# Optimization experiments

Measured on AMD Instinct MI355X. Metric: run time of the kernel, lower is better.

Reference implementation:

```python
import jax, jax.numpy as jnp
import numpy as np

NUM_HEADS = 16
HEAD_DIM = 32  # out_ch 512 / 16 heads

def _c(x):
    # last axis holds (real, imag) -> complex64
    return jax.lax.complex(x[..., 0], x[..., 1])

def setup_inputs() -> dict:
    key = jax.random.key(0)
    ks = jax.random.split(key, 9)
    B, S, C = 1, 2048, 512
    mk = lambda k, shp: jax.random.normal(k, shp, dtype=jnp.float32)
    return {
        "Q": mk(ks[0], (B, S, C, 2)),
        "V": mk(ks[1], (B, S, C, 2)),
        "K": mk(ks[2], (B, S, C, 2)),
        "Wq": mk(ks[3], (C, C, 2)) * (1.0 / np.sqrt(C)),
        "bq": mk(ks[4], (C, 2)) * 0.02,
        "Wk": mk(ks[5], (C, C, 2)) * (1.0 / np.sqrt(C)),
        "bk": mk(ks[6], (C, 2)) * 0.02,
        "Wv": mk(ks[7], (C, C, 2)) * (1.0 / np.sqrt(C)),
        "bv": mk(ks[8], (C, 2)) * 0.02,
    }

def _split_heads(x):
    B, S, D = x.shape
    return x.reshape(B, S, NUM_HEADS, HEAD_DIM).transpose(0, 2, 1, 3)  # [B,H,S,d]

def reference(Q, V, K, Wq, bq, Wk, bk, Wv, bv):
    Qc, Kc, Vc = _c(Q), _c(K), _c(V)
    # torch Linear: y = x @ W^T + b, W is [out, in]
    proj = lambda x, W, b: jnp.einsum('bsi,oi->bso', x, _c(W)) + _c(b)
    q = _split_heads(proj(Qc, Wq, bq))  # [B,H,S,d] complex64
    k = _split_heads(proj(Kc, Wk, bk))
    v = _split_heads(proj(Vc, Wv, bv))
    scores = jnp.einsum('bhqd,bhkd->bhqk', q, jnp.conj(k)) / np.sqrt(HEAD_DIM).astype(np.float32)
    weights = jax.nn.softmax(jnp.abs(scores), axis=-1)  # real [B,H,S,S]
    out = jnp.einsum('bhqk,bhkd->bhqd', weights.astype(v.dtype), v)  # complex
    B, H, S, d = out.shape
    out = out.transpose(0, 2, 1, 3).reshape(B, S, H * d)  # [B,S,out_ch]
    return jnp.stack([out.real, out.imag], axis=-1)  # [B,S,out_ch,2] float32
```

## Files before the change

### kernel.cpp

```cpp
#include <hip/hip_runtime.h>
#include <hip/hip_bf16.h>
#include <math.h>

#define S_LEN 2048
#define C_DIM 512
#define NH 16
#define HD 32
#define PLANE_U (NH * S_LEN * HD)
#define XF_OFF  (6*(size_t)PLANE_U)
#define WF_OFF  (12*(size_t)PLANE_U)
#define WPLF 262144

typedef __attribute__((ext_vector_type(8)))  short bf16x8;
typedef __attribute__((ext_vector_type(4)))  float f32x4;
typedef __attribute__((ext_vector_type(16))) float f32x16;
typedef __attribute__((ext_vector_type(4)))  unsigned int u32x4;

#if __has_builtin(__builtin_amdgcn_exp2f)
#define EXP2(x) __builtin_amdgcn_exp2f(x)
#else
#define EXP2(x) exp2f(x)
#endif

__device__ __forceinline__ unsigned int pk_bf16(float a, float b) {
    float2 f; f.x = a; f.y = b;
    __hip_bfloat162 t = __float22bfloat162_rn(f);
    return *reinterpret_cast<unsigned int*>(&t);
}

__global__ __launch_bounds__(256)
void xcvt(const float* __restrict__ Q, const float* __restrict__ K,
          const float* __restrict__ V, unsigned short* __restrict__ ws)
{
    const int tid  = blockIdx.x*256 + threadIdx.x;
    const int z    = tid >> 17;
    const int rem  = tid & 131071;
    const int kidx = rem >> 11;
    const int s    = rem & 2047;
    const int k    = kidx * 8;
    const float2* x2 = (const float2*)(z == 0 ? Q : (z == 1 ? K : V));
    const float4* s4 = (const float4*)(x2 + (size_t)s*C_DIM + k);
    float4 f0 = s4[0], f1 = s4[1], f2v = s4[2], f3 = s4[3];
    u32x4 rh, ih;
    rh[0] = pk_bf16(f0.x, f0.z); rh[1] = pk_bf16(f1.x, f1.z);
    rh[2] = pk_bf16(f2v.x, f2v.z); rh[3] = pk_bf16(f3.x, f3.z);
    ih[0] = pk_bf16(f0.y, f0.w); ih[1] = pk_bf16(f1.y, f1.w);
    ih[2] = pk_bf16(f2v.y, f2v.w); ih[3] = pk_bf16(f3.y, f3.w);
    const int sb = s >> 4, lr = s & 15, g = kidx & 3, kc = kidx >> 2;
    const size_t off = ((size_t)(sb*16 + kc)*64 + g*16 + lr)*8;
    unsigned short* base = ws + XF_OFF + (size_t)z*2*PLANE_U;
    *(u32x4*)&base[off]           = rh;
    *(u32x4*)&base[PLANE_U + off] = ih;
}

__global__ __launch_bounds__(256)
void wcvt(const float* __restrict__ Wq, const float* __restrict__ Wk,
          const float* __restrict__ Wv, unsigned short* __restrict__ ws)
{
    const int tid  = blockIdx.x*256 + threadIdx.x;
    const int z    = tid >> 15;
    const int rem  = tid & 32767;
    const int kidx = rem >> 9;
    const int o    = rem & 511;
    const int k    = kidx * 8;
    const float2* w2 = (const float2*)(z == 0 ? Wq : (z == 1 ? Wk : Wv));
    const float4* s4 = (const float4*)(w2 + (size_t)o*C_DIM + k);
    float4 f0 = s4[0], f1 = s4[1], f2v = s4[2], f3 = s4[3];
    u32x4 rh, ih;
    rh[0] = pk_bf16(f0.x, f0.z); rh[1] = pk_bf16(f1.x, f1.z);
    rh[2] = pk_bf16(f2v.x, f2v.z); rh[3] = pk_bf16(f3.x, f3.z);
    ih[0] = pk_bf16(f0.y, f0.w); ih[1] = pk_bf16(f1.y, f1.w);
    ih[2] = pk_bf16(f2v.y, f2v.w); ih[3] = pk_bf16(f3.y, f3.w);
    const int ob = o >> 4, lr = o & 15, g = kidx & 3, kc = kidx >> 2;
    const size_t off = ((size_t)(ob*16 + kc)*64 + g*16 + lr)*8;
    unsigned short* base = ws + WF_OFF + (size_t)z*2*WPLF;
    *(u32x4*)&base[off]       = rh;
    *(u32x4*)&base[WPLF + off] = ih;
}

__global__ __launch_bounds__(256)
void proj_mfma(const float* __restrict__ bq, const float* __restrict__ bk,
               const float* __restrict__ bv,
               unsigned short* __restrict__ ws)
{
    const int z = blockIdx.z;
    const float* b = (z == 0) ? bq : (z == 1 ? bk : bv);

    const int s0 = blockIdx.x * 32;
    const int o0 = blockIdx.y * 64;

    const unsigned short* xfR = ws + XF_OFF + (size_t)z*2*PLANE_U;
    const unsigned short* xfI = xfR + PLANE_U;
    const unsigned short* wfR = ws + WF_OFF + (size_t)z*2*WPLF;
    const unsigned short* wfI = wfR + WPLF;

    const int t    = threadIdx.x;
    const int wave = t >> 6;
    const int lane = t & 63;
    const int lr   = t & 15;
    const int g    = (t & 63) >> 4;

    const int ob = (o0 >> 4) + wave;
    const int sb = s0 >> 4;

    const f32x4 zf = {0.f,0.f,0.f,0.f};
    f32x4 accR[2], accI[2];
    #pragma unroll
    for (int i = 0; i < 2; ++i) { accR[i] = zf; accI[i] = zf; }

    for (int kc = 0; kc < 16; ++kc) {
        const size_t aoff = ((size_t)(ob*16 + kc)*64 + lane)*8;
        bf16x8 aRH = *(const bf16x8*)&wfR[aoff];
        bf16x8 aIH = *(const bf16x8*)&wfI[aoff];
        bf16x8 aIHn;
        #pragma unroll
        for (int j = 0; j < 4; ++j)
            ((unsigned int*)&aIHn)[j] = ((const unsigned int*)&aIH)[j] ^ 0x80008000u;

        const size_t b0 = ((size_t)(sb*16 + kc)*64 + lane)*8;
        const size_t b1 = ((size_t)((sb+1)*16 + kc)*64 + lane)*8;
        bf16x8 bRH0 = *(const bf16x8*)&xfR[b0];
        bf16x8 bIH0 = *(const bf16x8*)&xfI[b0];
        bf16x8 bRH1 = *(const bf16x8*)&xfR[b1];
        bf16x8 bIH1 = *(const bf16x8*)&xfI[b1];

        accR[0] = __builtin_amdgcn_mfma_f32_16x16x32_bf16(aRH,  bRH0, accR[0], 0,0,0);
        accR[0] = __builtin_amdgcn_mfma_f32_16x16x32_bf16(aIHn, bIH0, accR[0], 0,0,0);
        accI[0] = __builtin_amdgcn_mfma_f32_16x16x32_bf16(aRH,  bIH0, accI[0], 0,0,0);
        accI[0] = __builtin_amdgcn_mfma_f32_16x16x32_bf16(aIH,  bRH0, accI[0], 0,0,0);
        accR[1] = __builtin_amdgcn_mfma_f32_16x16x32_bf16(aRH,  bRH1, accR[1], 0,0,0);
        accR[1] = __builtin_amdgcn_mfma_f32_16x16x32_bf16(aIHn, bIH1, accR[1], 0,0,0);
        accI[1] = __builtin_amdgcn_mfma_f32_16x16x32_bf16(aRH,  bIH1, accI[1], 0,0,0);
        accI[1] = __builtin_amdgcn_mfma_f32_16x16x32_bf16(aIH,  bRH1, accI[1], 0,0,0);
    }

    const float2* b2 = (const float2*)b;
    const int obase = o0 + wave*16 + g*4;
    const int hh = obase >> 5, d0 = obase & 31;
    float bR[4], bI[4];
    #pragma unroll
    for (int r = 0; r < 4; ++r) { float2 bb = b2[obase + r]; bR[r] = bb.x; bI[r] = bb.y; }

    if (z == 0) {
        const float osc = 0.2550348677f;
        unsigned short* pr = ws;
        unsigned short* pi = pr + PLANE_U;
        #pragma unroll
        for (int tile = 0; tile < 2; ++tile) {
            int s = s0 + tile*16 + lr;
            size_t idx = ((size_t)hh*S_LEN + s)*HD + d0;
            uint2 pkR, pkI;
            pkR.x = pk_bf16((accR[tile][0]+bR[0])*osc, (accR[tile][1]+bR[1])*osc);
            pkR.y = pk_bf16((accR[tile][2]+bR[2])*osc, (accR[tile][3]+bR[3])*osc);
            pkI.x = pk_bf16((accI[tile][0]+bI[0])*osc, (accI[tile][1]+bI[1])*osc);
            pkI.y = pk_bf16((accI[tile][2]+bI[2])*osc, (accI[tile][3]+bI[3])*osc);
            *(uint2*)&pr[idx] = pkR;
            *(uint2*)&pi[idx] = pkI;
        }
    } else if (z == 1) {
        unsigned short* kf = ws + 2*(size_t)PLANE_U;
        const int frag_re = (d0 >= 16) ? 1 : 0;
        const int bsel    = (d0 & 15) >> 3;
        const int e       = d0 & 7;
        #pragma unroll
        for (int tile = 0; tile < 2; ++tile) {
            int s = s0 + tile*16 + lr;
            int c = s >> 5;
            int i = s & 31;
            int r = (i & ~12) | ((i & 4) << 1) | ((i & 8) >> 1);
            int lane2 = bsel*32 + r;
            size_t base = ((size_t)(hh*64 + c)*4)*512 + lane2*8 + e;
            uint2 pkR, pkI;
            pkR.x = pk_bf16(accR[tile][0]+bR[0], accR[tile][1]+bR[1]);
            pkR.y = pk_bf16(accR[tile][2]+bR[2], accR[tile][3]+bR[3]);
            pkI.x = pk_bf16(accI[tile][0]+bI[0], accI[tile][1]+bI[1]);
            pkI.y = pk_bf16(accI[tile][2]+bI[2], accI[tile][3]+bI[3]);
            *(uint2*)&kf[base + (size_t)frag_re*512]     = pkR;
            *(uint2*)&kf[base + (size_t)(2+frag_re)*512] = pkI;
        }
    } else {
        unsigned short* vf = ws + 4*(size_t)PLANE_U;
        const int bsel = lr >> 3;
        const int e    = lr & 7;
        #pragma unroll
        for (int tile = 0; tile < 2; ++tile) {
            int s = s0 + tile*16 + lr;
            const int c       = s >> 5;
            const int frag_re = (s & 31) >= 16 ? 1 : 0;
            const size_t cb   = ((size_t)(hh*64 + c)*4)*512;
            #pragma unroll
            for (int r = 0; r < 4; ++r) {
                int lane2 = bsel*32 + d0 + r;
                size_t base = cb + (size_t)lane2*8 + e;
                vf[base + (size_t)frag_re*512]     =
                    (unsigned short)pk_bf16(accR[tile][r]+bR[r], 0.f);
                vf[base + (size_t)(2+frag_re)*512] =
                    (unsigned short)pk_bf16(accI[tile][r]+bI[r], 0.f);
            }
        }
    }
}

#define RROW 33

__global__ __launch_bounds__(256, 4)
void attn_mfma(const unsigned short* __restrict__ ws, float* __restrict__ out)
{
    const int bid   = blockIdx.x;
    const int h     = bid & (NH - 1);
    const int qblk  = bid >> 4;
    const int wave  = threadIdx.x >> 6;
    const int l     = threadIdx.x & 63;
    const int q     = l & 31;
    const int b     = l >> 5;

    const unsigned short* qr = ws + 0*(size_t)PLANE_U + (size_t)h*S_LEN*HD;
    const unsigned short* qi = ws + 1*(size_t)PLANE_U + (size_t)h*S_LEN*HD;
    const unsigned short* kf = ws + 2*(size_t)PLANE_U + ((size_t)h << 17);
    const unsigned short* vf = ws + 4*(size_t)PLANE_U + ((size_t)h << 17);

    const int q0 = qblk * 32;

    bf16x8 bQr_lo = *(const bf16x8*)&qr[(size_t)(q0 + q)*HD + b*8];
    bf16x8 bQr_hi = *(const bf16x8*)&qr[(size_t)(q0 + q)*HD + 16 + b*8];
    bf16x8 bQi_lo = *(const bf16x8*)&qi[(size_t)(q0 + q)*HD + b*8];
    bf16x8 bQi_hi = *(const bf16x8*)&qi[(size_t)(q0 + q)*HD + 16 + b*8];

    __shared__ __align__(16) float2 red[2*32*RROW];

    f32x16 accR, accI;
    #pragma unroll
    for (int r = 0; r < 16; ++r) { accR[r] = 0.f; accI[r] = 0.f; }
    float lsum = 0.f;

    const f32x16 z16 = {0,0,0,0,0,0,0,0,0,0,0,0,0,0,0,0};
    const int kbeg = wave * 512;
    for (int k0 = kbeg; k0 < kbeg + 512; k0 += 32) {
        const size_t fb = (size_t)(k0 >> 5) * 2048 + l*8;

        bf16x8 aVr_lo = *(const bf16x8*)&vf[fb];
        bf16x8 aVr_hi = *(const bf16x8*)&vf[fb + 512];
        bf16x8 aVi_lo = *(const bf16x8*)&vf[fb + 1024];
        bf16x8 aVi_hi = *(const bf16x8*)&vf[fb + 1536];

        bf16x8 aKr_lo = *(const bf16x8*)&kf[fb];
        bf16x8 aKr_hi = *(const bf16x8*)&kf[fb + 512];
        bf16x8 aKi_lo = *(const bf16x8*)&kf[fb + 1024];
        bf16x8 aKi_hi = *(const bf16x8*)&kf[fb + 1536];
        bf16x8 aKin_lo, aKin_hi;
        #pragma unroll
        for (int j = 0; j < 4; ++j) {
            ((unsigned int*)&aKin_lo)[j] = ((const unsigned int*)&aKi_lo)[j] ^ 0x80008000u;
            ((unsigned int*)&aKin_hi)[j] = ((const unsigned int*)&aKi_hi)[j] ^ 0x80008000u;
        }
        f32x16 sR = __builtin_amdgcn_mfma_f32_32x32x16_bf16(aKr_lo,  bQr_lo, z16, 0, 0, 0);
        f32x16 sI = __builtin_amdgcn_mfma_f32_32x32x16_bf16(aKin_lo, bQr_lo, z16, 0, 0, 0);
        sR = __builtin_amdgcn_mfma_f32_32x32x16_bf16(aKr_hi,  bQr_hi, sR, 0, 0, 0);
        sI = __builtin_amdgcn_mfma_f32_32x32x16_bf16(aKin_hi, bQr_hi, sI, 0, 0, 0);
        sR = __builtin_amdgcn_mfma_f32_32x32x16_bf16(aKi_lo,  bQi_lo, sR, 0, 0, 0);
        sI = __builtin_amdgcn_mfma_f32_32x32x16_bf16(aKr_lo,  bQi_lo, sI, 0, 0, 0);
        sR = __builtin_amdgcn_mfma_f32_32x32x16_bf16(aKi_hi,  bQi_hi, sR, 0, 0, 0);
        sI = __builtin_amdgcn_mfma_f32_32x32x16_bf16(aKr_hi,  bQi_hi, sI, 0, 0, 0);

        bf16x8 bP1, bP2;
        unsigned int* p1 = (unsigned int*)&bP1;
        unsigned int* p2 = (unsigned int*)&bP2;
        #pragma unroll
        for (int r2 = 0; r2 < 8; ++r2) {
            int r = 2*r2;
            float v0 = EXP2(__builtin_amdgcn_sqrtf(fmaf(sR[r],   sR[r],   sI[r]*sI[r])));
            float v1 = EXP2(__builtin_amdgcn_sqrtf(fmaf(sR[r+1], sR[r+1], sI[r+1]*sI[r+1])));
            lsum += v0 + v1;
            if (r2 < 4) p1[r2]     = pk_bf16(v0, v1);
            else        p2[r2 - 4] = pk_bf16(v0, v1);
        }
        accR = __builtin_amdgcn_mfma_f32_32x32x16_bf16(aVr_lo, bP1, accR, 0, 0, 0);
        accI = __builtin_amdgcn_mfma_f32_32x32x16_bf16(aVi_lo, bP1, accI, 0, 0, 0);
        accR = __builtin_amdgcn_mfma_f32_32x32x16_bf16(aVr_hi, bP2, accR, 0, 0, 0);
        accI = __builtin_amdgcn_mfma_f32_32x32x16_bf16(aVi_hi, bP2, accI, 0, 0, 0);
    }

    lsum += __shfl_xor(lsum, 32);

    const int rrow = ((wave & 1) * 32 + q) * RROW;
    __syncthreads();
    if (wave < 2) {
        #pragma unroll
        for (int r = 0; r < 16; ++r) {
            int d = (r & 3) + 8*(r >> 2) + 4*b;
            red[rrow + d] = make_float2(accR[r], accI[r]);
        }
        if (b == 0) red[rrow + 32].x = lsum;
    }
    __syncthreads();
    if (wave >= 2) {
        #pragma unroll
        for (int r = 0; r < 16; ++r) {
            int d = (r & 3) + 8*(r >> 2) + 4*b;
            float2 v = red[rrow + d];
            v.x += accR[r]; v.y += accI[r];
            red[rrow + d] = v;
        }
        if (b == 0) red[rrow + 32].x += lsum;
    }
    __syncthreads();

    {
        const int i  = threadIdx.x;
        const int oq = i >> 3;
        const int d0 = (i & 7) * 4;
        float sl = red[oq*RROW + 32].x + red[(32 + oq)*RROW + 32].x;
        float inv = 1.0f / sl;
        float2* o2 = (float2*)out;
        #pragma unroll
        for (int dd = 0; dd < 4; ++dd) {
            int d = d0 + dd;
            float2 v0 = red[oq*RROW + d];
            float2 v1 = red[(32 + oq)*RROW + d];
            o2[(size_t)(q0 + oq)*C_DIM + h*HD + d] =
                make_float2((v0.x + v1.x)*inv, (v0.y + v1.y)*inv);
        }
    }
}

extern "C" void kernel_launch(void* const* d_in, const int* in_sizes, int n_in,
                              void* d_out, int out_size, void* d_ws, size_t ws_size,
                              hipStream_t stream)
{
    const float* Q  = (const float*)d_in[0];
    const float* V  = (const float*)d_in[1];
    const float* K  = (const float*)d_in[2];
    const float* Wq = (const float*)d_in[3];
    const float* bq = (const float*)d_in[4];
    const float* Wk = (const float*)d_in[5];
    const float* bk = (const float*)d_in[6];
    const float* Wv = (const float*)d_in[7];
    const float* bv = (const float*)d_in[8];
    unsigned short* ws = (unsigned short*)d_ws;
    float* out = (float*)d_out;

    xcvt<<<1536, 256, 0, stream>>>(Q, K, V, ws);
    wcvt<<<384, 256, 0, stream>>>(Wq, Wk, Wv, ws);
    proj_mfma<<<dim3(S_LEN/32, C_DIM/64, 3), 256, 0, stream>>>(bq, bk, bv, ws);
    attn_mfma<<<dim3(64*NH), 256, 0, stream>>>(ws, out);
}
```

Baseline: 78.21 us.

## Merge conversion kernels, prefetch weights in projection, set MFMA priority in attention

The separate input and weight fp32-to-bf16 conversion kernels become one launch, with the block index choosing the path, which saves one kernel launch and its tail. The projection loop is fully unrolled and loads the next weight fragment one step early (register double-buffering) so load latency overlaps with the MFMAs. The attention loop raises wave priority around its MFMA groups with s_setprio so the matrix unit stays busier while other waves run the exp/sqrt work. These are independent ideas and add some register pressure.

```diff
diff --git a/kernel.cpp b/kernel.cpp
--- a/kernel.cpp
+++ b/kernel.cpp
@@ -29,53 +29,52 @@
 }
 
 __global__ __launch_bounds__(256)
-void xcvt(const float* __restrict__ Q, const float* __restrict__ K,
-          const float* __restrict__ V, unsigned short* __restrict__ ws)
+void xwcvt(const float* __restrict__ Q, const float* __restrict__ K,
+           const float* __restrict__ V,
+           const float* __restrict__ Wq, const float* __restrict__ Wk,
+           const float* __restrict__ Wv, unsigned short* __restrict__ ws)
 {
-    const int tid  = blockIdx.x*256 + threadIdx.x;
-    const int z    = tid >> 17;
-    const int rem  = tid & 131071;
-    const int kidx = rem >> 11;
-    const int s    = rem & 2047;
-    const int k    = kidx * 8;
-    const float2* x2 = (const float2*)(z == 0 ? Q : (z == 1 ? K : V));
-    const float4* s4 = (const float4*)(x2 + (size_t)s*C_DIM + k);
-    float4 f0 = s4[0], f1 = s4[1], f2v = s4[2], f3 = s4[3];
-    u32x4 rh, ih;
-    rh[0] = pk_bf16(f0.x, f0.z); rh[1] = pk_bf16(f1.x, f1.z);
-    rh[2] = pk_bf16(f2v.x, f2v.z); rh[3] = pk_bf16(f3.x, f3.z);
-    ih[0] = pk_bf16(f0.y, f0.w); ih[1] = pk_bf16(f1.y, f1.w);
-    ih[2] = pk_bf16(f2v.y, f2v.w); ih[3] = pk_bf16(f3.y, f3.w);
-    const int sb = s >> 4, lr = s & 15, g = kidx & 3, kc = kidx >> 2;
-    const size_t off = ((size_t)(sb*16 + kc)*64 + g*16 + lr)*8;
-    unsigned short* base = ws + XF_OFF + (size_t)z*2*PLANE_U;
-    *(u32x4*)&base[off]           = rh;
-    *(u32x4*)&base[PLANE_U + off] = ih;
-}
-
-__global__ __launch_bounds__(256)
-void wcvt(const float* __restrict__ Wq, const float* __restrict__ Wk,
-          const float* __restrict__ Wv, unsigned short* __restrict__ ws)
-{
-    const int tid  = blockIdx.x*256 + threadIdx.x;
-    const int z    = tid >> 15;
-    const int rem  = tid & 32767;
-    const int kidx = rem >> 9;
-    const int o    = rem & 511;
-    const int k    = kidx * 8;
-    const float2* w2 = (const float2*)(z == 0 ? Wq : (z == 1 ? Wk : Wv));
-    const float4* s4 = (const float4*)(w2 + (size_t)o*C_DIM + k);
-    float4 f0 = s4[0], f1 = s4[1], f2v = s4[2], f3 = s4[3];
-    u32x4 rh, ih;
-    rh[0] = pk_bf16(f0.x, f0.z); rh[1] = pk_bf16(f1.x, f1.z);
-    rh[2] = pk_bf16(f2v.x, f2v.z); rh[3] = pk_bf16(f3.x, f3.z);
-    ih[0] = pk_bf16(f0.y, f0.w); ih[1] = pk_bf16(f1.y, f1.w);
-    ih[2] = pk_bf16(f2v.y, f2v.w); ih[3] = pk_bf16(f3.y, f3.w);
-    const int ob = o >> 4, lr = o & 15, g = kidx & 3, kc = kidx >> 2;
-    const size_t off = ((size_t)(ob*16 + kc)*64 + g*16 + lr)*8;
-    unsigned short* base = ws + WF_OFF + (size_t)z*2*WPLF;
-    *(u32x4*)&base[off]       = rh;
-    *(u32x4*)&base[WPLF + off] = ih;
+    if (blockIdx.x < 1536) {
+        const int tid  = blockIdx.x*256 + threadIdx.x;
+        const int z    = tid >> 17;
+        const int rem  = tid & 131071;
+        const int kidx = rem >> 11;
+        const int s    = rem & 2047;
+        const int k    = kidx * 8;
+        const float2* x2 = (const float2*)(z == 0 ? Q : (z == 1 ? K : V));
+        const float4* s4 = (const float4*)(x2 + (size_t)s*C_DIM + k);
+        float4 f0 = s4[0], f1 = s4[1], f2v = s4[2], f3 = s4[3];
+        u32x4 rh, ih;
+        rh[0] = pk_bf16(f0.x, f0.z); rh[1] = pk_bf16(f1.x, f1.z);
+        rh[2] = pk_bf16(f2v.x, f2v.z); rh[3] = pk_bf16(f3.x, f3.z);
+        ih[0] = pk_bf16(f0.y, f0.w); ih[1] = pk_bf16(f1.y, f1.w);
+        ih[2] = pk_bf16(f2v.y, f2v.w); ih[3] = pk_bf16(f3.y, f3.w);
+        const int sb = s >> 4, lr = s & 15, g = kidx & 3, kc = kidx >> 2;
+        const size_t off = ((size_t)(sb*16 + kc)*64 + g*16 + lr)*8;
+        unsigned short* base = ws + XF_OFF + (size_t)z*2*PLANE_U;
+        *(u32x4*)&base[off]           = rh;
+        *(u32x4*)&base[PLANE_U + off] = ih;
+    } else {
+        const int tid  = (blockIdx.x - 1536)*256 + threadIdx.x;
+        const int z    = tid >> 15;
+        const int rem  = tid & 32767;
+        const int kidx = rem >> 9;
+        const int o    = rem & 511;
+        const int k    = kidx * 8;
+        const float2* w2 = (const float2*)(z == 0 ? Wq : (z == 1 ? Wk : Wv));
+        const float4* s4 = (const float4*)(w2 + (size_t)o*C_DIM + k);
+        float4 f0 = s4[0], f1 = s4[1], f2v = s4[2], f3 = s4[3];
+        u32x4 rh, ih;
+        rh[0] = pk_bf16(f0.x, f0.z); rh[1] = pk_bf16(f1.x, f1.z);
+        rh[2] = pk_bf16(f2v.x, f2v.z); rh[3] = pk_bf16(f3.x, f3.z);
+        ih[0] = pk_bf16(f0.y, f0.w); ih[1] = pk_bf16(f1.y, f1.w);
+        ih[2] = pk_bf16(f2v.y, f2v.w); ih[3] = pk_bf16(f3.y, f3.w);
+        const int ob = o >> 4, lr = o & 15, g = kidx & 3, kc = kidx >> 2;
+        const size_t off = ((size_t)(ob*16 + kc)*64 + g*16 + lr)*8;
+        unsigned short* base = ws + WF_OFF + (size_t)z*2*WPLF;
+        *(u32x4*)&base[off]        = rh;
+        *(u32x4*)&base[WPLF + off] = ih;
+    }
 }
 
 __global__ __launch_bounds__(256)
@@ -108,10 +107,12 @@
     #pragma unroll
     for (int i = 0; i < 2; ++i) { accR[i] = zf; accI[i] = zf; }
 
+    size_t aoff = ((size_t)(ob*16)*64 + lane)*8;
+    bf16x8 aRH = *(const bf16x8*)&wfR[aoff];
+    bf16x8 aIH = *(const bf16x8*)&wfI[aoff];
+
+    #pragma unroll
     for (int kc = 0; kc < 16; ++kc) {
-        const size_t aoff = ((size_t)(ob*16 + kc)*64 + lane)*8;
-        bf16x8 aRH = *(const bf16x8*)&wfR[aoff];
-        bf16x8 aIH = *(const bf16x8*)&wfI[aoff];
         bf16x8 aIHn;
         #pragma unroll
         for (int j = 0; j < 4; ++j)
@@ -124,14 +125,21 @@
         bf16x8 bRH1 = *(const bf16x8*)&xfR[b1];
         bf16x8 bIH1 = *(const bf16x8*)&xfI[b1];
 
-        accR[0] = __builtin_amdgcn_mfma_f32_16x16x32_bf16(aRH,  bRH0, accR[0], 0,0,0);
+        bf16x8 aRHc = aRH, aIHc = aIH;
+        if (kc < 15) {
+            const size_t an = ((size_t)(ob*16 + kc + 1)*64 + lane)*8;
+            aRH = *(const bf16x8*)&wfR[an];
+            aIH = *(const bf16x8*)&wfI[an];
+        }
+
+        accR[0] = __builtin_amdgcn_mfma_f32_16x16x32_bf16(aRHc, bRH0, accR[0], 0,0,0);
         accR[0] = __builtin_amdgcn_mfma_f32_16x16x32_bf16(aIHn, bIH0, accR[0], 0,0,0);
-        accI[0] = __builtin_amdgcn_mfma_f32_16x16x32_bf16(aRH,  bIH0, accI[0], 0,0,0);
-        accI[0] = __builtin_amdgcn_mfma_f32_16x16x32_bf16(aIH,  bRH0, accI[0], 0,0,0);
-        accR[1] = __builtin_amdgcn_mfma_f32_16x16x32_bf16(aRH,  bRH1, accR[1], 0,0,0);
+        accI[0] = __builtin_amdgcn_mfma_f32_16x16x32_bf16(aRHc, bIH0, accI[0], 0,0,0);
+        accI[0] = __builtin_amdgcn_mfma_f32_16x16x32_bf16(aIHc, bRH0, accI[0], 0,0,0);
+        accR[1] = __builtin_amdgcn_mfma_f32_16x16x32_bf16(aRHc, bRH1, accR[1], 0,0,0);
         accR[1] = __builtin_amdgcn_mfma_f32_16x16x32_bf16(aIHn, bIH1, accR[1], 0,0,0);
-        accI[1] = __builtin_amdgcn_mfma_f32_16x16x32_bf16(aRH,  bIH1, accI[1], 0,0,0);
-        accI[1] = __builtin_amdgcn_mfma_f32_16x16x32_bf16(aIH,  bRH1, accI[1], 0,0,0);
+        accI[1] = __builtin_amdgcn_mfma_f32_16x16x32_bf16(aRHc, bIH1, accI[1], 0,0,0);
+        accI[1] = __builtin_amdgcn_mfma_f32_16x16x32_bf16(aIHc, bRH1, accI[1], 0,0,0);
     }
 
     const float2* b2 = (const float2*)b;
@@ -253,6 +261,7 @@
             ((unsigned int*)&aKin_lo)[j] = ((const unsigned int*)&aKi_lo)[j] ^ 0x80008000u;
             ((unsigned int*)&aKin_hi)[j] = ((const unsigned int*)&aKi_hi)[j] ^ 0x80008000u;
         }
+        __builtin_amdgcn_s_setprio(1);
         f32x16 sR = __builtin_amdgcn_mfma_f32_32x32x16_bf16(aKr_lo,  bQr_lo, z16, 0, 0, 0);
         f32x16 sI = __builtin_amdgcn_mfma_f32_32x32x16_bf16(aKin_lo, bQr_lo, z16, 0, 0, 0);
         sR = __builtin_amdgcn_mfma_f32_32x32x16_bf16(aKr_hi,  bQr_hi, sR, 0, 0, 0);
@@ -261,6 +270,7 @@
         sI = __builtin_amdgcn_mfma_f32_32x32x16_bf16(aKr_lo,  bQi_lo, sI, 0, 0, 0);
         sR = __builtin_amdgcn_mfma_f32_32x32x16_bf16(aKi_hi,  bQi_hi, sR, 0, 0, 0);
         sI = __builtin_amdgcn_mfma_f32_32x32x16_bf16(aKr_hi,  bQi_hi, sI, 0, 0, 0);
+        __builtin_amdgcn_s_setprio(0);
 
         bf16x8 bP1, bP2;
         unsigned int* p1 = (unsigned int*)&bP1;
@@ -274,10 +284,12 @@
             if (r2 < 4) p1[r2]     = pk_bf16(v0, v1);
             else        p2[r2 - 4] = pk_bf16(v0, v1);
         }
+        __builtin_amdgcn_s_setprio(1);
         accR = __builtin_amdgcn_mfma_f32_32x32x16_bf16(aVr_lo, bP1, accR, 0, 0, 0);
         accI = __builtin_amdgcn_mfma_f32_32x32x16_bf16(aVi_lo, bP1, accI, 0, 0, 0);
         accR = __builtin_amdgcn_mfma_f32_32x32x16_bf16(aVr_hi, bP2, accR, 0, 0, 0);
         accI = __builtin_amdgcn_mfma_f32_32x32x16_bf16(aVi_hi, bP2, accI, 0, 0, 0);
+        __builtin_amdgcn_s_setprio(0);
     }
 
     lsum += __shfl_xor(lsum, 32);
@@ -339,8 +351,7 @@
     unsigned short* ws = (unsigned short*)d_ws;
     float* out = (float*)d_out;
 
-    xcvt<<<1536, 256, 0, stream>>>(Q, K, V, ws);
-    wcvt<<<384, 256, 0, stream>>>(Wq, Wk, Wv, ws);
+    xwcvt<<<1920, 256, 0, stream>>>(Q, K, V, Wq, Wk, Wv, ws);
     proj_mfma<<<dim3(S_LEN/32, C_DIM/64, 3), 256, 0, stream>>>(bq, bk, bv, ws);
     attn_mfma<<<dim3(64*NH), 256, 0, stream>>>(ws, out);
 }
```

Result: faster. 72.84 us, median of 2 (-6.9%).
